# Performance work log

Measured on AMD Instinct MI355X. Metric: run time of the kernel, lower is better.

## Reference

```python
import jax, jax.numpy as jnp
import numpy as np

N = 50000      # nodes
E = 800000     # edges (avg degree 16)
IN = 128       # in_features
H = 4          # num_heads
OUT = 32       # out_features per head
NEG_SLOPE = 0.2


def setup_inputs() -> dict:
    key = jax.random.key(0)
    k1, k2, k3, k4 = jax.random.split(key, 4)
    h = jax.random.normal(k1, (N, IN), dtype=jnp.float32)
    edge_index = jax.random.randint(k2, (2, E), 0, N, dtype=jnp.int32)
    # xavier-ish init scales
    W = jax.random.normal(k3, (H, IN, OUT), dtype=jnp.float32) * np.float32(np.sqrt(2.0 / (IN + OUT)))
    a = jax.random.normal(k4, (H, 2 * OUT), dtype=jnp.float32) * np.float32(np.sqrt(2.0 / (2 * OUT)))
    return {"h": h, "edge_index": edge_index, "W": W, "a": a}


def reference(h, edge_index, W, a):
    src, dst = edge_index[0], edge_index[1]
    # project per head: [N, H, OUT]
    h_proj = jnp.einsum('ni,hio->nho', h, W)
    # score = leaky_relu(a . [Wh_src || Wh_dst]) ; split a to avoid materializing the concat
    a_src, a_dst = a[:, :OUT], a[:, OUT:]
    s_src = jnp.einsum('nho,ho->nh', h_proj, a_src)   # [N, H]
    s_dst = jnp.einsum('nho,ho->nh', h_proj, a_dst)   # [N, H]
    score = jax.nn.leaky_relu(s_src[src] + s_dst[dst], negative_slope=NEG_SLOPE)  # [E, H]
    # sparse softmax over incoming edges of each dst node
    smax = jax.ops.segment_max(score, dst, num_segments=N)          # [N, H]
    smax = jnp.where(jnp.isfinite(smax), smax, jnp.float32(-1e9))   # nodes with no in-edges
    score_exp = jnp.exp(score - smax[dst])                          # [E, H]
    denom = jax.ops.segment_sum(score_exp, dst, num_segments=N)     # [N, H]
    denom = jnp.maximum(denom, jnp.float32(1e-16))
    alpha = score_exp / denom[dst]                                  # [E, H]
    # weighted aggregation (dropout is identity in eval mode)
    h_src = h_proj[src]                                             # [E, H, OUT]
    h_out = jax.ops.segment_sum(alpha[:, :, None] * h_src, dst, num_segments=N)  # [N, H, OUT]
    h_out = h_out.reshape(N, H * OUT)  # concat=True
    return jax.nn.elu(h_out)
```

## Files before the change

### kernel.cpp

```cpp
#include <hip/hip_runtime.h>

#define NEG_SLOPE 0.2f
#define BCAP 8192

typedef __attribute__((ext_vector_type(8))) short short8;
typedef __attribute__((ext_vector_type(4))) float floatx4;

__device__ __forceinline__ unsigned f2bf(float x) {
  unsigned u = __float_as_uint(x);
  unsigned r = ((u >> 16) & 1u) + 0x7fffu;
  return (u + r) >> 16;
}
__device__ __forceinline__ float bf2f(unsigned hi16) {
  return __uint_as_float(hi16 << 16);
}

__global__ __launch_bounds__(256) void k_prep(const float* __restrict__ W,
                                              uint4* __restrict__ gWf,
                                              int* __restrict__ bcur, int NB2) {
  if (blockIdx.x == 0 && threadIdx.x < NB2) bcur[threadIdx.x] = 0;
  const int u = blockIdx.x * 256 + threadIdx.x;
  if (u >= 2048) return;
  int ln = u & 63;
  int kc = (u >> 6) & 3;
  int ct = u >> 8;
  int n = ct * 16 + (ln & 15);
  int kb = kc * 32 + (ln >> 4) * 8;
  int head = n >> 5;
  const float* src = W + head * 4096 + (size_t)kb * 32 + (n & 31);
  unsigned hi[4], lo[4];
#pragma unroll
  for (int jj = 0; jj < 4; ++jj) {
    float w0 = src[(2 * jj) * 32];
    float w1 = src[(2 * jj + 1) * 32];
    unsigned h0 = f2bf(w0), h1 = f2bf(w1);
    unsigned l0 = f2bf(w0 - bf2f(h0)), l1 = f2bf(w1 - bf2f(h1));
    hi[jj] = h0 | (h1 << 16);
    lo[jj] = l0 | (l1 << 16);
  }
  gWf[u] = make_uint4(hi[0], hi[1], hi[2], hi[3]);
  gWf[2048 + u] = make_uint4(lo[0], lo[1], lo[2], lo[3]);
}

__global__ __launch_bounds__(256) void k_gemm(const float* __restrict__ h,
                                              const uint4* __restrict__ gWf,
                                              const float* __restrict__ a,
                                              unsigned short* __restrict__ hp16,
                                              float* __restrict__ ssrc,
                                              float* __restrict__ sdst, int N) {
  __shared__ unsigned lds_u[16384];
  const int tid = threadIdx.x;
  const int lane = tid & 63;
  const int wv = tid >> 6;
  const int quad = lane >> 4;
  const int l16 = lane & 15;

  for (int u = tid; u < 4096; u += 256)
    *(uint4*)&lds_u[u * 4] = gWf[u];

  const int row0 = blockIdx.x * 64;
  const int r = row0 + wv * 16 + l16;
  short8 Ah[4], Al[4];
#pragma unroll
  for (int kc = 0; kc < 4; ++kc) {
    float v[8];
    if (r < N) {
      float4 fa = *(const float4*)&h[(size_t)r * 128 + kc * 32 + quad * 8];
      float4 fb = *(const float4*)&h[(size_t)r * 128 + kc * 32 + quad * 8 + 4];
      v[0] = fa.x; v[1] = fa.y; v[2] = fa.z; v[3] = fa.w;
      v[4] = fb.x; v[5] = fb.y; v[6] = fb.z; v[7] = fb.w;
    } else {
#pragma unroll
      for (int j = 0; j < 8; ++j) v[j] = 0.f;
    }
#pragma unroll
    for (int j = 0; j < 8; ++j) {
      unsigned hi = f2bf(v[j]);
      Ah[kc][j] = (short)hi;
      Al[kc][j] = (short)f2bf(v[j] - bf2f(hi));
    }
  }
  __syncthreads();

  floatx4 C[8];
#pragma unroll
  for (int ct = 0; ct < 8; ++ct) {
    floatx4 c = {0.f, 0.f, 0.f, 0.f};
#pragma unroll
    for (int kc = 0; kc < 4; ++kc) {
      int bidx = ((ct * 4 + kc) * 64 + lane) * 4;
      short8 Bh, Bl;
      *(uint4*)&Bh = *(const uint4*)&lds_u[bidx];
      *(uint4*)&Bl = *(const uint4*)&lds_u[8192 + bidx];
      c = __builtin_amdgcn_mfma_f32_16x16x32_bf16(Ah[kc], Bh, c, 0, 0, 0);
      c = __builtin_amdgcn_mfma_f32_16x16x32_bf16(Al[kc], Bh, c, 0, 0, 0);
      c = __builtin_amdgcn_mfma_f32_16x16x32_bf16(Ah[kc], Bl, c, 0, 0, 0);
    }
    C[ct] = c;
  }
  __syncthreads();

  float* epi = (float*)lds_u;
#pragma unroll
  for (int ct = 0; ct < 8; ++ct) {
#pragma unroll
    for (int reg = 0; reg < 4; ++reg) {
      int rr = wv * 16 + quad * 4 + reg;
      epi[rr * 132 + ct * 16 + l16] = C[ct][reg];
    }
  }
  __syncthreads();

  const int row_l = tid >> 2;
  const int hh = tid & 3;
  const int rg = row0 + row_l;
  if (rg < N) {
    const float* rowp = &epi[row_l * 132 + hh * 32];
    float ss = 0.f, sd = 0.f;
    unsigned pka[16];
#pragma unroll
    for (int e = 0; e < 8; ++e) {
      float4 c4 = *(const float4*)&rowp[e * 4];
      float4 as = *(const float4*)&a[hh * 64 + e * 4];
      float4 ad = *(const float4*)&a[hh * 64 + 32 + e * 4];
      ss += c4.x * as.x + c4.y * as.y + c4.z * as.z + c4.w * as.w;
      sd += c4.x * ad.x + c4.y * ad.y + c4.z * ad.z + c4.w * ad.w;
      pka[e * 2] = f2bf(c4.x) | (f2bf(c4.y) << 16);
      pka[e * 2 + 1] = f2bf(c4.z) | (f2bf(c4.w) << 16);
    }
    unsigned short* dst = &hp16[(size_t)rg * 128 + hh * 32];
    *(uint4*)(dst) = make_uint4(pka[0], pka[1], pka[2], pka[3]);
    *(uint4*)(dst + 8) = make_uint4(pka[4], pka[5], pka[6], pka[7]);
    *(uint4*)(dst + 16) = make_uint4(pka[8], pka[9], pka[10], pka[11]);
    *(uint4*)(dst + 24) = make_uint4(pka[12], pka[13], pka[14], pka[15]);
    ssrc[(size_t)rg * 4 + hh] = ss;
    sdst[(size_t)rg * 4 + hh] = sd;
  }
}

__global__ __launch_bounds__(256) void k_bin(const int* __restrict__ ei,
                                             int* __restrict__ bcur,
                                             uint2* __restrict__ gpairs,
                                             int E, int NB2) {
  __shared__ uint2 stage[4096];
  __shared__ int cnt[256], start[256], cur[256], gbase[256];
  __shared__ int lds[256];
  const int tid = threadIdx.x;
  const int e0 = blockIdx.x * 4096;
  for (int i = tid; i < NB2; i += 256) cnt[i] = 0;
  __syncthreads();
  int sarr[16], darr[16];
#pragma unroll
  for (int j = 0; j < 16; ++j) {
    int e = e0 + j * 256 + tid;
    if (e < E) {
      sarr[j] = ei[e];
      darr[j] = ei[E + e];
      atomicAdd(&cnt[darr[j] >> 8], 1);
    } else {
      darr[j] = -1;
    }
  }
  __syncthreads();
  {
    int s = (tid < NB2) ? cnt[tid] : 0;
    lds[tid] = s;
    __syncthreads();
    for (int off = 1; off < 256; off <<= 1) {
      int t = (tid >= off) ? lds[tid - off] : 0;
      __syncthreads();
      lds[tid] += t;
      __syncthreads();
    }
    if (tid < NB2) {
      start[tid] = lds[tid] - s;
      cur[tid] = lds[tid] - s;
      gbase[tid] = s ? atomicAdd(&bcur[tid], s) : 0;
    }
  }
  __syncthreads();
#pragma unroll
  for (int j = 0; j < 16; ++j) {
    if (darr[j] >= 0) {
      int b = darr[j] >> 8;
      int pos = atomicAdd(&cur[b], 1);
      stage[pos] = make_uint2((unsigned)sarr[j], (unsigned)darr[j]);
    }
  }
  __syncthreads();
  const int total = start[NB2 - 1] + cnt[NB2 - 1];
  for (int u = tid; u < total; u += 256) {
    uint2 pr = stage[u];
    int b = (int)(pr.y >> 8);
    gpairs[(size_t)b * BCAP + gbase[b] + (u - start[b])] = pr;
  }
}

__global__ __launch_bounds__(256) void k_build(const int* __restrict__ bcur,
                                               const uint2* __restrict__ gpairs,
                                               int* __restrict__ csr_src,
                                               int2* __restrict__ offs2, int N) {
  __shared__ int cnt2[256], start2[256], cur2[256];
  __shared__ int lds[256];
  __shared__ int srcsort[BCAP];
  const int tid = threadIdx.x;
  const int b = blockIdx.x;
  const size_t base = (size_t)b * BCAP;
  const int size = bcur[b];
  const int d0 = b << 8;
  const int ndst = min(256, N - d0);
  cnt2[tid] = 0;
  __syncthreads();
  for (int u = tid; u < size; u += 256)
    atomicAdd(&cnt2[(int)gpairs[base + u].y - d0], 1);
  __syncthreads();
  {
    int s = cnt2[tid];
    lds[tid] = s;
    __syncthreads();
    for (int off = 1; off < 256; off <<= 1) {
      int t = (tid >= off) ? lds[tid - off] : 0;
      __syncthreads();
      lds[tid] += t;
      __syncthreads();
    }
    start2[tid] = lds[tid] - s;
    cur2[tid] = lds[tid] - s;
  }
  __syncthreads();
  for (int u = tid; u < size; u += 256) {
    uint2 pr = gpairs[base + u];
    int pos = atomicAdd(&cur2[(int)pr.y - d0], 1);
    srcsort[pos] = (int)pr.x;
  }
  __syncthreads();
  for (int u = tid; u < size; u += 256) csr_src[base + u] = srcsort[u];
  if (tid < ndst) {
    int beg = (int)base + start2[tid];
    offs2[d0 + tid] = make_int2(beg, beg + cnt2[tid]);
  }
}

__global__ __launch_bounds__(256) void k_agg(const int2* __restrict__ offs2,
                                             const int* __restrict__ csr_src,
                                             const float* __restrict__ ssrc,
                                             const float* __restrict__ sdst,
                                             const uint4* __restrict__ hp4,
                                             float* __restrict__ out, int N) {
  const int t = blockIdx.x * 256 + threadIdx.x;
  const int d = t >> 4;
  if (d >= N) return;
  const int l = threadIdx.x & 15;
  const int hh = l >> 2;
  const int2 be = offs2[d];
  const int beg = be.x, end = be.y;
  const float sdh = sdst[(size_t)d * 4 + hh];

  float den[4] = {0.f, 0.f, 0.f, 0.f};
  float acc[8];
#pragma unroll
  for (int j = 0; j < 8; ++j) acc[j] = 0.f;

  int p = beg;
  for (; p + 3 < end; p += 4) {
    int s[4];
    float sc[4];
    uint4 v[4];
#pragma unroll
    for (int q = 0; q < 4; ++q) s[q] = csr_src[p + q];
#pragma unroll
    for (int q = 0; q < 4; ++q) {
      sc[q] = ssrc[(size_t)s[q] * 4 + hh] + sdh;
      v[q] = hp4[(size_t)s[q] * 16 + l];
    }
#pragma unroll
    for (int q = 0; q < 4; ++q) {
      float x = sc[q];
      x = x >= 0.f ? x : NEG_SLOPE * x;
      float w = __expf(x);
      den[q] += w;
      acc[0] = fmaf(w, bf2f(v[q].x & 0xffffu), acc[0]);
      acc[1] = fmaf(w, bf2f(v[q].x >> 16), acc[1]);
      acc[2] = fmaf(w, bf2f(v[q].y & 0xffffu), acc[2]);
      acc[3] = fmaf(w, bf2f(v[q].y >> 16), acc[3]);
      acc[4] = fmaf(w, bf2f(v[q].z & 0xffffu), acc[4]);
      acc[5] = fmaf(w, bf2f(v[q].z >> 16), acc[5]);
      acc[6] = fmaf(w, bf2f(v[q].w & 0xffffu), acc[6]);
      acc[7] = fmaf(w, bf2f(v[q].w >> 16), acc[7]);
    }
  }
  for (; p < end; ++p) {
    int s0 = csr_src[p];
    float sc0 = ssrc[(size_t)s0 * 4 + hh] + sdh;
    uint4 v0 = hp4[(size_t)s0 * 16 + l];
    sc0 = sc0 >= 0.f ? sc0 : NEG_SLOPE * sc0;
    float w0 = __expf(sc0);
    den[0] += w0;
    acc[0] = fmaf(w0, bf2f(v0.x & 0xffffu), acc[0]);
    acc[1] = fmaf(w0, bf2f(v0.x >> 16), acc[1]);
    acc[2] = fmaf(w0, bf2f(v0.y & 0xffffu), acc[2]);
    acc[3] = fmaf(w0, bf2f(v0.y >> 16), acc[3]);
    acc[4] = fmaf(w0, bf2f(v0.z & 0xffffu), acc[4]);
    acc[5] = fmaf(w0, bf2f(v0.z >> 16), acc[5]);
    acc[6] = fmaf(w0, bf2f(v0.w & 0xffffu), acc[6]);
    acc[7] = fmaf(w0, bf2f(v0.w >> 16), acc[7]);
  }
  float rden = 1.f / fmaxf((den[0] + den[1]) + (den[2] + den[3]), 1e-16f);
  float o[8];
#pragma unroll
  for (int j = 0; j < 8; ++j) {
    float x = acc[j] * rden;
    o[j] = x > 0.f ? x : expm1f(x);
  }
  float* dst = &out[(size_t)d * 128 + l * 8];
  *(float4*)dst = make_float4(o[0], o[1], o[2], o[3]);
  *(float4*)(dst + 4) = make_float4(o[4], o[5], o[6], o[7]);
}

extern "C" void kernel_launch(void* const* d_in, const int* in_sizes, int n_in,
                              void* d_out, int out_size, void* d_ws, size_t ws_size,
                              hipStream_t stream) {
  const float* h = (const float*)d_in[0];
  const int* ei = (const int*)d_in[1];
  const float* W = (const float*)d_in[2];
  const float* a = (const float*)d_in[3];
  float* out = (float*)d_out;
  const int N = in_sizes[0] / 128;
  const int E = in_sizes[1] / 2;
  const int NB2 = (N + 255) >> 8;
  const int NB1 = (E + 4095) / 4096;

  char* ws = (char*)d_ws;
  uint4* gWf = (uint4*)ws;
  unsigned short* hp16 = (unsigned short*)(gWf + 4096);
  uint2* gpairs = (uint2*)(hp16 + (size_t)N * 128);
  int2* offs2 = (int2*)(gpairs + (size_t)NB2 * BCAP);
  float* ssrc = (float*)(offs2 + N);
  float* sdst = ssrc + (size_t)N * 4;
  int* bcur = (int*)(sdst + (size_t)N * 4);
  int* csr_src = bcur + NB2;

  k_prep<<<8, 256, 0, stream>>>(W, gWf, bcur, NB2);
  k_gemm<<<(N + 63) / 64, 256, 0, stream>>>(h, gWf, a, hp16, ssrc, sdst, N);
  k_bin<<<NB1, 256, 0, stream>>>(ei, bcur, gpairs, E, NB2);
  k_build<<<NB2, 256, 0, stream>>>(bcur, gpairs, csr_src, offs2, N);
  k_agg<<<(N * 16 + 255) / 256, 256, 0, stream>>>(offs2, csr_src, ssrc, sdst,
                                                  (const uint4*)hp16, out, N);
}
```

Baseline: 159.7 us.

## Fuse edge binning into GEMM kernel and precompute edge attention weights in build

Merges the edge-binning pass into the projection GEMM kernel: the first NB1 blocks bin edges before doing their GEMM rows, which removes one launch and overlaps the two phases. The CSR build kernel now also computes exp(leaky_relu(ssrc+sdst)) per edge for all four heads and stores it as float4 in CSR order. The aggregation kernel then reads these weights directly instead of doing a random ssrc gather and an exp per edge. This costs an extra 16 bytes per edge of writes and reads, and lengthens the binning blocks inside the GEMM grid. The GEMM path in the fused kernel is otherwise unchanged.

Measured after the change: 159.3 us. About the same (-0.2%).

```diff
diff --git a/kernel.cpp b/kernel.cpp
--- a/kernel.cpp
+++ b/kernel.cpp
@@ -45,11 +45,72 @@
 __global__ __launch_bounds__(256) void k_gemm(const float* __restrict__ h,
                                               const uint4* __restrict__ gWf,
                                               const float* __restrict__ a,
+                                              const int* __restrict__ ei,
+                                              int* __restrict__ bcur,
+                                              uint2* __restrict__ gpairs,
                                               unsigned short* __restrict__ hp16,
                                               float* __restrict__ ssrc,
-                                              float* __restrict__ sdst, int N) {
+                                              float* __restrict__ sdst,
+                                              int N, int E, int NB1, int NB2) {
   __shared__ unsigned lds_u[16384];
   const int tid = threadIdx.x;
+
+  if (blockIdx.x < NB1) {
+    uint2* stage = (uint2*)lds_u;
+    int* cnt = (int*)&lds_u[8192];
+    int* start = (int*)&lds_u[8448];
+    int* cur = (int*)&lds_u[8704];
+    int* gbase = (int*)&lds_u[8960];
+    int* scn = (int*)&lds_u[9216];
+    const int e0 = blockIdx.x * 4096;
+    for (int i = tid; i < NB2; i += 256) cnt[i] = 0;
+    __syncthreads();
+    int sarr[16], darr[16];
+#pragma unroll
+    for (int j = 0; j < 16; ++j) {
+      int e = e0 + j * 256 + tid;
+      if (e < E) {
+        sarr[j] = ei[e];
+        darr[j] = ei[E + e];
+        atomicAdd(&cnt[darr[j] >> 8], 1);
+      } else {
+        darr[j] = -1;
+      }
+    }
+    __syncthreads();
+    int s = (tid < NB2) ? cnt[tid] : 0;
+    scn[tid] = s;
+    __syncthreads();
+    for (int off = 1; off < 256; off <<= 1) {
+      int t = (tid >= off) ? scn[tid - off] : 0;
+      __syncthreads();
+      scn[tid] += t;
+      __syncthreads();
+    }
+    if (tid < NB2) {
+      start[tid] = scn[tid] - s;
+      cur[tid] = scn[tid] - s;
+      gbase[tid] = s ? atomicAdd(&bcur[tid], s) : 0;
+    }
+    __syncthreads();
+#pragma unroll
+    for (int j = 0; j < 16; ++j) {
+      if (darr[j] >= 0) {
+        int b = darr[j] >> 8;
+        int pos = atomicAdd(&cur[b], 1);
+        stage[pos] = make_uint2((unsigned)sarr[j], (unsigned)darr[j]);
+      }
+    }
+    __syncthreads();
+    const int total = start[NB2 - 1] + cnt[NB2 - 1];
+    for (int u = tid; u < total; u += 256) {
+      uint2 pr = stage[u];
+      int b = (int)(pr.y >> 8);
+      gpairs[(size_t)b * BCAP + gbase[b] + (u - start[b])] = pr;
+    }
+    __syncthreads();
+  }
+
   const int lane = tid & 63;
   const int wv = tid >> 6;
   const int quad = lane >> 4;
@@ -138,67 +199,12 @@
   }
 }
 
-__global__ __launch_bounds__(256) void k_bin(const int* __restrict__ ei,
-                                             int* __restrict__ bcur,
-                                             uint2* __restrict__ gpairs,
-                                             int E, int NB2) {
-  __shared__ uint2 stage[4096];
-  __shared__ int cnt[256], start[256], cur[256], gbase[256];
-  __shared__ int lds[256];
-  const int tid = threadIdx.x;
-  const int e0 = blockIdx.x * 4096;
-  for (int i = tid; i < NB2; i += 256) cnt[i] = 0;
-  __syncthreads();
-  int sarr[16], darr[16];
-#pragma unroll
-  for (int j = 0; j < 16; ++j) {
-    int e = e0 + j * 256 + tid;
-    if (e < E) {
-      sarr[j] = ei[e];
-      darr[j] = ei[E + e];
-      atomicAdd(&cnt[darr[j] >> 8], 1);
-    } else {
-      darr[j] = -1;
-    }
-  }
-  __syncthreads();
-  {
-    int s = (tid < NB2) ? cnt[tid] : 0;
-    lds[tid] = s;
-    __syncthreads();
-    for (int off = 1; off < 256; off <<= 1) {
-      int t = (tid >= off) ? lds[tid - off] : 0;
-      __syncthreads();
-      lds[tid] += t;
-      __syncthreads();
-    }
-    if (tid < NB2) {
-      start[tid] = lds[tid] - s;
-      cur[tid] = lds[tid] - s;
-      gbase[tid] = s ? atomicAdd(&bcur[tid], s) : 0;
-    }
-  }
-  __syncthreads();
-#pragma unroll
-  for (int j = 0; j < 16; ++j) {
-    if (darr[j] >= 0) {
-      int b = darr[j] >> 8;
-      int pos = atomicAdd(&cur[b], 1);
-      stage[pos] = make_uint2((unsigned)sarr[j], (unsigned)darr[j]);
-    }
-  }
-  __syncthreads();
-  const int total = start[NB2 - 1] + cnt[NB2 - 1];
-  for (int u = tid; u < total; u += 256) {
-    uint2 pr = stage[u];
-    int b = (int)(pr.y >> 8);
-    gpairs[(size_t)b * BCAP + gbase[b] + (u - start[b])] = pr;
-  }
-}
-
 __global__ __launch_bounds__(256) void k_build(const int* __restrict__ bcur,
                                                const uint2* __restrict__ gpairs,
+                                               const float* __restrict__ ssrc,
+                                               const float* __restrict__ sdst,
                                                int* __restrict__ csr_src,
+                                               float4* __restrict__ escore,
                                                int2* __restrict__ offs2, int N) {
   __shared__ int cnt2[256], start2[256], cur2[256];
   __shared__ int lds[256];
@@ -230,8 +236,19 @@
   __syncthreads();
   for (int u = tid; u < size; u += 256) {
     uint2 pr = gpairs[base + u];
-    int pos = atomicAdd(&cur2[(int)pr.y - d0], 1);
-    srcsort[pos] = (int)pr.x;
+    int d = (int)pr.y;
+    int pos = atomicAdd(&cur2[d - d0], 1);
+    int s = (int)pr.x;
+    srcsort[pos] = s;
+    float4 sv = *(const float4*)&ssrc[(size_t)s * 4];
+    float4 dv = *(const float4*)&sdst[(size_t)d * 4];
+    float4 w;
+    float x;
+    x = sv.x + dv.x; x = x >= 0.f ? x : NEG_SLOPE * x; w.x = __expf(x);
+    x = sv.y + dv.y; x = x >= 0.f ? x : NEG_SLOPE * x; w.y = __expf(x);
+    x = sv.z + dv.z; x = x >= 0.f ? x : NEG_SLOPE * x; w.z = __expf(x);
+    x = sv.w + dv.w; x = x >= 0.f ? x : NEG_SLOPE * x; w.w = __expf(x);
+    escore[base + pos] = w;
   }
   __syncthreads();
   for (int u = tid; u < size; u += 256) csr_src[base + u] = srcsort[u];
@@ -243,8 +260,7 @@
 
 __global__ __launch_bounds__(256) void k_agg(const int2* __restrict__ offs2,
                                              const int* __restrict__ csr_src,
-                                             const float* __restrict__ ssrc,
-                                             const float* __restrict__ sdst,
+                                             const float* __restrict__ escore,
                                              const uint4* __restrict__ hp4,
                                              float* __restrict__ out, int N) {
   const int t = blockIdx.x * 256 + threadIdx.x;
@@ -254,7 +270,6 @@
   const int hh = l >> 2;
   const int2 be = offs2[d];
   const int beg = be.x, end = be.y;
-  const float sdh = sdst[(size_t)d * 4 + hh];
 
   float den[4] = {0.f, 0.f, 0.f, 0.f};
   float acc[8];
@@ -264,37 +279,32 @@
   int p = beg;
   for (; p + 3 < end; p += 4) {
     int s[4];
-    float sc[4];
+    float w[4];
     uint4 v[4];
 #pragma unroll
     for (int q = 0; q < 4; ++q) s[q] = csr_src[p + q];
 #pragma unroll
     for (int q = 0; q < 4; ++q) {
-      sc[q] = ssrc[(size_t)s[q] * 4 + hh] + sdh;
+      w[q] = escore[(size_t)(p + q) * 4 + hh];
       v[q] = hp4[(size_t)s[q] * 16 + l];
     }
 #pragma unroll
     for (int q = 0; q < 4; ++q) {
-      float x = sc[q];
-      x = x >= 0.f ? x : NEG_SLOPE * x;
-      float w = __expf(x);
-      den[q] += w;
-      acc[0] = fmaf(w, bf2f(v[q].x & 0xffffu), acc[0]);
-      acc[1] = fmaf(w, bf2f(v[q].x >> 16), acc[1]);
-      acc[2] = fmaf(w, bf2f(v[q].y & 0xffffu), acc[2]);
-      acc[3] = fmaf(w, bf2f(v[q].y >> 16), acc[3]);
-      acc[4] = fmaf(w, bf2f(v[q].z & 0xffffu), acc[4]);
-      acc[5] = fmaf(w, bf2f(v[q].z >> 16), acc[5]);
-      acc[6] = fmaf(w, bf2f(v[q].w & 0xffffu), acc[6]);
-      acc[7] = fmaf(w, bf2f(v[q].w >> 16), acc[7]);
+      den[q] += w[q];
+      acc[0] = fmaf(w[q], bf2f(v[q].x & 0xffffu), acc[0]);
+      acc[1] = fmaf(w[q], bf2f(v[q].x >> 16), acc[1]);
+      acc[2] = fmaf(w[q], bf2f(v[q].y & 0xffffu), acc[2]);
+      acc[3] = fmaf(w[q], bf2f(v[q].y >> 16), acc[3]);
+      acc[4] = fmaf(w[q], bf2f(v[q].z & 0xffffu), acc[4]);
+      acc[5] = fmaf(w[q], bf2f(v[q].z >> 16), acc[5]);
+      acc[6] = fmaf(w[q], bf2f(v[q].w & 0xffffu), acc[6]);
+      acc[7] = fmaf(w[q], bf2f(v[q].w >> 16), acc[7]);
     }
   }
   for (; p < end; ++p) {
     int s0 = csr_src[p];
-    float sc0 = ssrc[(size_t)s0 * 4 + hh] + sdh;
+    float w0 = escore[(size_t)p * 4 + hh];
     uint4 v0 = hp4[(size_t)s0 * 16 + l];
-    sc0 = sc0 >= 0.f ? sc0 : NEG_SLOPE * sc0;
-    float w0 = __expf(sc0);
     den[0] += w0;
     acc[0] = fmaf(w0, bf2f(v0.x & 0xffffu), acc[0]);
     acc[1] = fmaf(w0, bf2f(v0.x >> 16), acc[1]);
@@ -329,21 +339,23 @@
   const int E = in_sizes[1] / 2;
   const int NB2 = (N + 255) >> 8;
   const int NB1 = (E + 4095) / 4096;
+  const int NBG = max((N + 63) / 64, NB1);
 
   char* ws = (char*)d_ws;
   uint4* gWf = (uint4*)ws;
   unsigned short* hp16 = (unsigned short*)(gWf + 4096);
   uint2* gpairs = (uint2*)(hp16 + (size_t)N * 128);
-  int2* offs2 = (int2*)(gpairs + (size_t)NB2 * BCAP);
+  float4* escore = (float4*)(gpairs + (size_t)NB2 * BCAP);
+  int2* offs2 = (int2*)(escore + (size_t)NB2 * BCAP);
   float* ssrc = (float*)(offs2 + N);
   float* sdst = ssrc + (size_t)N * 4;
   int* bcur = (int*)(sdst + (size_t)N * 4);
   int* csr_src = bcur + NB2;
 
   k_prep<<<8, 256, 0, stream>>>(W, gWf, bcur, NB2);
-  k_gemm<<<(N + 63) / 64, 256, 0, stream>>>(h, gWf, a, hp16, ssrc, sdst, N);
-  k_bin<<<NB1, 256, 0, stream>>>(ei, bcur, gpairs, E, NB2);
-  k_build<<<NB2, 256, 0, stream>>>(bcur, gpairs, csr_src, offs2, N);
-  k_agg<<<(N * 16 + 255) / 256, 256, 0, stream>>>(offs2, csr_src, ssrc, sdst,
+  k_gemm<<<NBG, 256, 0, stream>>>(h, gWf, a, ei, bcur, gpairs, hp16, ssrc, sdst,
+                                  N, E, NB1, NB2);
+  k_build<<<NB2, 256, 0, stream>>>(bcur, gpairs, ssrc, sdst, csr_src, escore, offs2, N);
+  k_agg<<<(N * 16 + 255) / 256, 256, 0, stream>>>(offs2, csr_src, (const float*)escore,
                                                   (const uint4*)hp16, out, N);
 }
```
